# Kernel tuning notes

Measured on AMD Instinct MI355X. Metric: run time of the kernel, lower is better.

The kernel has to match this reference:

```python
import jax, jax.numpy as jnp
import numpy as np

# Problem dims (production MPPI-style rollout batch)
B, H, L, S, O = 512, 32, 7, 5, 8  # batch, horizon, links, spheres/link, world objs
DIST_THRESHOLD = 0.1


def setup_inputs() -> dict:
    key = jax.random.key(0)
    ks = jax.random.split(key, 6)
    # forward args
    link_pos_seq = jax.random.normal(ks[0], (B, H, L, 3), dtype=jnp.float32) * 0.5
    link_rot_seq = jax.random.normal(ks[1], (B, H, L, 3, 3), dtype=jnp.float32)
    # learned/config params: robot collision spheres (link frame) + world sphere primitives
    sphere_offsets = jax.random.normal(ks[2], (L, S, 3), dtype=jnp.float32) * 0.1
    sphere_radii = jax.random.uniform(ks[3], (L, S), dtype=jnp.float32, minval=0.02, maxval=0.08)
    obj_centers = jax.random.normal(ks[4], (O, 3), dtype=jnp.float32) * 0.6
    obj_radii = jax.random.uniform(ks[5], (O,), dtype=jnp.float32, minval=0.05, maxval=0.3)
    weight = jnp.asarray(1.0, dtype=jnp.float32)
    return {
        "link_pos_seq": link_pos_seq,
        "link_rot_seq": link_rot_seq,
        "sphere_offsets": sphere_offsets,
        "sphere_radii": sphere_radii,
        "obj_centers": obj_centers,
        "obj_radii": obj_radii,
        "weight": weight,
    }


def reference(link_pos_seq, link_rot_seq, sphere_offsets, sphere_radii,
              obj_centers, obj_radii, weight):
    b, h, l, _ = link_pos_seq.shape
    n = b * h
    pos = link_pos_seq.reshape(n, l, 3)          # [N,L,3]
    rot = link_rot_seq.reshape(n, l, 3, 3)       # [N,L,3,3]
    # transform link-frame collision spheres into world frame: c = R @ o + p
    centers = jnp.einsum('nlij,lsj->nlsi', rot, sphere_offsets) + pos[:, :, None, :]  # [N,L,S,3]
    # sphere-vs-world-sphere signed distance (positive = penetration)
    diff = centers[:, :, :, None, :] - obj_centers[None, None, None, :, :]  # [N,L,S,O,3]
    d = jnp.sqrt(jnp.sum(diff * diff, axis=-1))                             # [N,L,S,O]
    signed = (sphere_radii[None, :, :, None] + obj_radii[None, None, None, :]) - d
    dist = jnp.max(signed, axis=(2, 3)).reshape(b, h, l)  # worst sphere/obj per link
    # clamp-scale-sum-weight chain from forward()
    dist = jnp.clip(dist + DIST_THRESHOLD, 0.0, 0.2) / 0.25
    cost = weight * jnp.sum(dist, axis=-1)  # [B,H]
    return cost
```

## Files before the change

### kernel.cpp

```cpp
#include <hip/hip_runtime.h>

#define BB 512
#define HH 32
#define LL 7
#define SS 5
#define OO 8
#define NN (BB * HH)
#define DIST_THRESHOLD 0.1f

typedef float f4 __attribute__((ext_vector_type(4)));
typedef float f2 __attribute__((ext_vector_type(2)));

__global__ __launch_bounds__(256)
void PrimitiveCollisionCost_19533511262442_kernel(
    const float* __restrict__ pos,
    const float* __restrict__ rot,
    const float* __restrict__ off,
    const float* __restrict__ srad,
    const float* __restrict__ oc,
    const float* __restrict__ orad,
    const float* __restrict__ weight,
    float* __restrict__ out)
{
    const int t = blockIdx.x * blockDim.x + threadIdx.x;
    const int n = t >> 3;
    const int l = t & 7;

    float dist = 0.0f;

    if (l < LL) {
        const float* posn = pos + (size_t)n * (LL * 3) + l * 3;
        const float* rotn = rot + (size_t)n * (LL * 9) + l * 9;

        const f2    p01 = *(const f2*)(posn);
        const float pz  = posn[2];
        const f4    ra  = *(const f4*)(rotn);
        const f4    rb  = *(const f4*)(rotn + 4);
        const float r22 = rotn[8];

        const float px = p01.x, py = p01.y;
        const float r00 = ra.x, r01 = ra.y, r02 = ra.z, r10 = ra.w;
        const float r11 = rb.x, r12 = rb.y, r20 = rb.z, r21 = rb.w;

        float cx[SS], cy[SS], cz[SS], rs[SS];
#pragma unroll
        for (int s = 0; s < SS; ++s) {
            const float ox = off[(l * SS + s) * 3 + 0];
            const float oy = off[(l * SS + s) * 3 + 1];
            const float oz = off[(l * SS + s) * 3 + 2];
            rs[s] = srad[l * SS + s];
            cx[s] = r00 * ox + r01 * oy + r02 * oz + px;
            cy[s] = r10 * ox + r11 * oy + r12 * oz + py;
            cz[s] = r20 * ox + r21 * oy + r22 * oz + pz;
        }

        float best[SS];
#pragma unroll
        for (int s = 0; s < SS; ++s) best[s] = -1e30f;

#pragma unroll
        for (int o = 0; o < OO; ++o) {
            const float ocx = oc[o * 3 + 0];
            const float ocy = oc[o * 3 + 1];
            const float ocz = oc[o * 3 + 2];
            const float ro  = orad[o];
#pragma unroll
            for (int s = 0; s < SS; ++s) {
                const float dx = cx[s] - ocx;
                const float dy = cy[s] - ocy;
                const float dz = cz[s] - ocz;
                const float d  = __builtin_amdgcn_sqrtf(dx * dx + dy * dy + dz * dz);
                best[s] = fmaxf(best[s], (rs[s] + ro) - d);
            }
        }

        float b = best[0];
#pragma unroll
        for (int s = 1; s < SS; ++s) b = fmaxf(b, best[s]);

        dist = fminf(fmaxf(b + DIST_THRESHOLD, 0.0f), 0.2f) * 4.0f;
    }

    dist += __shfl_xor(dist, 1, 64);
    dist += __shfl_xor(dist, 2, 64);
    dist += __shfl_xor(dist, 4, 64);

    if (l == 0) {
        out[n] = weight[0] * dist;
    }
}

extern "C" void kernel_launch(void* const* d_in, const int* in_sizes, int n_in,
                              void* d_out, int out_size, void* d_ws, size_t ws_size,
                              hipStream_t stream) {
    const float* pos    = (const float*)d_in[0];
    const float* rot    = (const float*)d_in[1];
    const float* off    = (const float*)d_in[2];
    const float* srad   = (const float*)d_in[3];
    const float* oc     = (const float*)d_in[4];
    const float* orad   = (const float*)d_in[5];
    const float* weight = (const float*)d_in[6];
    float* out = (float*)d_out;

    constexpr int block = 256;
    constexpr int grid  = (NN * 8) / block;

    PrimitiveCollisionCost_19533511262442_kernel<<<grid, block, 0, stream>>>(
        pos, rot, off, srad, oc, orad, weight, out);
}
```

Before: 70.70 us.

## Spread each rollout across a full wavefront, one lane per link-object pair

Each rollout step now gets 64 lanes, one per link and world object, instead of 8 lanes with one per link. Each lane computes five sphere-object distances instead of forty. Lanes take a max-reduction across objects and then a sum across links using xor shuffles. This shortens each thread's serial chain and launches eight times as many waves to raise occupancy and hide latency. The cost is that each lane recomputes its link's sphere transforms and reloads pos and rot, so that work is repeated eight times per link.

```diff
diff --git a/kernel.cpp b/kernel.cpp
--- a/kernel.cpp
+++ b/kernel.cpp
@@ -22,9 +22,11 @@
     const float* __restrict__ weight,
     float* __restrict__ out)
 {
-    const int t = blockIdx.x * blockDim.x + threadIdx.x;
-    const int n = t >> 3;
-    const int l = t & 7;
+    const int t    = blockIdx.x * blockDim.x + threadIdx.x;
+    const int n    = t >> 6;
+    const int lane = t & 63;
+    const int o    = lane & 7;
+    const int l    = lane >> 3;
 
     float dist = 0.0f;
 
@@ -42,50 +44,43 @@
         const float r00 = ra.x, r01 = ra.y, r02 = ra.z, r10 = ra.w;
         const float r11 = rb.x, r12 = rb.y, r20 = rb.z, r21 = rb.w;
 
-        float cx[SS], cy[SS], cz[SS], rs[SS];
+        const float ocx = oc[o * 3 + 0];
+        const float ocy = oc[o * 3 + 1];
+        const float ocz = oc[o * 3 + 2];
+        const float ro  = orad[o];
+
+        float best = -1e30f;
+
 #pragma unroll
         for (int s = 0; s < SS; ++s) {
             const float ox = off[(l * SS + s) * 3 + 0];
             const float oy = off[(l * SS + s) * 3 + 1];
             const float oz = off[(l * SS + s) * 3 + 2];
-            rs[s] = srad[l * SS + s];
-            cx[s] = r00 * ox + r01 * oy + r02 * oz + px;
-            cy[s] = r10 * ox + r11 * oy + r12 * oz + py;
-            cz[s] = r20 * ox + r21 * oy + r22 * oz + pz;
+            const float rs = srad[l * SS + s];
+
+            const float cx = r00 * ox + r01 * oy + r02 * oz + px;
+            const float cy = r10 * ox + r11 * oy + r12 * oz + py;
+            const float cz = r20 * ox + r21 * oy + r22 * oz + pz;
+
+            const float dx = cx - ocx;
+            const float dy = cy - ocy;
+            const float dz = cz - ocz;
+            const float d  = __builtin_amdgcn_sqrtf(dx * dx + dy * dy + dz * dz);
+            best = fmaxf(best, (rs + ro) - d);
         }
 
-        float best[SS];
-#pragma unroll
-        for (int s = 0; s < SS; ++s) best[s] = -1e30f;
+        best = fmaxf(best, __shfl_xor(best, 1, 64));
+        best = fmaxf(best, __shfl_xor(best, 2, 64));
+        best = fmaxf(best, __shfl_xor(best, 4, 64));
 
-#pragma unroll
-        for (int o = 0; o < OO; ++o) {
-            const float ocx = oc[o * 3 + 0];
-            const float ocy = oc[o * 3 + 1];
-            const float ocz = oc[o * 3 + 2];
-            const float ro  = orad[o];
-#pragma unroll
-            for (int s = 0; s < SS; ++s) {
-                const float dx = cx[s] - ocx;
-                const float dy = cy[s] - ocy;
-                const float dz = cz[s] - ocz;
-                const float d  = __builtin_amdgcn_sqrtf(dx * dx + dy * dy + dz * dz);
-                best[s] = fmaxf(best[s], (rs[s] + ro) - d);
-            }
-        }
-
-        float b = best[0];
-#pragma unroll
-        for (int s = 1; s < SS; ++s) b = fmaxf(b, best[s]);
-
-        dist = fminf(fmaxf(b + DIST_THRESHOLD, 0.0f), 0.2f) * 4.0f;
+        dist = fminf(fmaxf(best + DIST_THRESHOLD, 0.0f), 0.2f) * 4.0f;
     }
 
-    dist += __shfl_xor(dist, 1, 64);
-    dist += __shfl_xor(dist, 2, 64);
-    dist += __shfl_xor(dist, 4, 64);
+    dist += __shfl_xor(dist, 8, 64);
+    dist += __shfl_xor(dist, 16, 64);
+    dist += __shfl_xor(dist, 32, 64);
 
-    if (l == 0) {
+    if (lane == 0) {
         out[n] = weight[0] * dist;
     }
 }
@@ -103,7 +98,7 @@
     float* out = (float*)d_out;
 
     constexpr int block = 256;
-    constexpr int grid  = (NN * 8) / block;
+    constexpr int grid  = (NN * 64) / block;
 
     PrimitiveCollisionCost_19533511262442_kernel<<<grid, block, 0, stream>>>(
         pos, rot, off, srad, oc, orad, weight, out);
```

After: 74.11 us. +4.8%, slower.
